# Optimization experiments

Hardware: AMD Instinct MI355X
Metric: run time of the kernel (lower is better)

The kernel has to match this reference:

```python
import jax, jax.numpy as jnp
import numpy as np

B, T, DM, H, DK, DV = 2, 2048, 1024, 16, 64, 64


def setup_inputs() -> dict:
    key = jax.random.key(0)
    k = jax.random.split(key, 7)
    std_k = np.float32(1.0 / np.sqrt(DK))
    std_v = np.float32(1.0 / np.sqrt(DV))
    return {
        "xq": jax.random.normal(k[0], (B, T, DM), jnp.float32),
        "xk": jax.random.normal(k[1], (B, T, DM), jnp.float32),
        "xv": jax.random.normal(k[2], (B, T, DM), jnp.float32),
        "mask": jnp.ones((B, T), jnp.float32),  # padding mask: 1 = keep
        "w_q": jax.random.normal(k[3], (H, DM, DK), jnp.float32) * std_k,
        "w_k": jax.random.normal(k[4], (H, DM, DK), jnp.float32) * std_k,
        "w_v": jax.random.normal(k[5], (H, DM, DV), jnp.float32) * std_v,
        "w_o": jax.random.normal(k[6], (H * DV, DM), jnp.float32) * np.float32(1.0 / np.sqrt(H * DV)),
        "b_o": jnp.zeros((DM,), jnp.float32),
    }


def reference(xq, xk, xv, mask, w_q, w_k, w_v, w_o, b_o):
    d_k = w_q.shape[-1]
    # per-head projections: [B,T,DM] x [H,DM,DK] -> [B,H,T,DK]
    q = jnp.einsum('bsd,hdk->bhsk', xq, w_q)
    kk = jnp.einsum('btd,hdk->bhtk', xk, w_k)
    v = jnp.einsum('btd,hdv->bhtv', xv, w_v)
    # NOTE: source divides by d_k (not sqrt(d_k)) -- kept faithful
    scores = jnp.einsum('bhsk,bhtk->bhst', q, kk) / jnp.float32(d_k)
    # _padding_mask: multiply by mask broadcast over key dim, then any exact
    # zero (masked OR coincidentally zero score) becomes -inf -- kept faithful
    masked = scores * mask[:, None, None, :]
    scores = jnp.where(masked == 0.0, -jnp.inf, masked)
    attn = jax.nn.softmax(scores, axis=-1)
    out = jnp.einsum('bhst,bhtv->bhsv', attn, v)  # [B,H,T,DV]
    b, h, t, dv = out.shape
    concat = out.transpose(0, 2, 1, 3).reshape(b, t, h * dv)
    return concat @ w_o + b_o
```

## Files before the change

### kernel.cpp

```cpp
#include <hip/hip_runtime.h>
#include <hip/hip_bf16.h>


typedef __attribute__((ext_vector_type(8))) short short8;
typedef __attribute__((ext_vector_type(4))) short short4v;
typedef __attribute__((ext_vector_type(4))) float f32x4;
typedef __attribute__((ext_vector_type(4))) int i32x4;

__device__ __forceinline__ short f2bf(float f) {
  union { float f; unsigned u; } v; v.f = f;
  unsigned r = v.u + 0x7FFFu + ((v.u >> 16) & 1u);
  return (short)(r >> 16);
}

#define GLD_LDS(g, l) __builtin_amdgcn_global_load_lds( \
    (const __attribute__((address_space(1))) void*)(g), \
    (__attribute__((address_space(3))) void*)(l), 16, 0, 0)

__global__ __launch_bounds__(256) void prep_all(
    const float* __restrict__ xq, const float* __restrict__ xk,
    const float* __restrict__ xv, const float* __restrict__ wq,
    const float* __restrict__ wk, const float* __restrict__ wv,
    const float* __restrict__ wo,
    short* __restrict__ Xb, short* __restrict__ Wall, short* __restrict__ Wot)
{
  const int bx = blockIdx.x, tid = threadIdx.x;
  __shared__ float Lt[64][65];
  if (bx < 6144) {
    int z = bx >> 11;
    const float* x = z == 0 ? xq : (z == 1 ? xk : xv);
    size_t i = ((size_t)(bx & 2047) * 256 + tid) * 8;
    f32x4 f0 = *(const f32x4*)(x + i);
    f32x4 f1 = *(const f32x4*)(x + i + 4);
    short8 s;
#pragma unroll
    for (int j = 0; j < 4; j++) { s[j] = f2bf(f0[j]); s[4 + j] = f2bf(f1[j]); }
    *(short8*)(Xb + (size_t)z * 4194304 + i) = s;
  } else if (bx < 6912) {
    int bz = bx - 6144;
    int z = bz >> 8, inner = bz & 255;
    const float* w = z == 0 ? wq : (z == 1 ? wk : wv);
    short* Wt = Wall + (size_t)z * 1048576;
    int h = inner >> 4, d0 = (inner & 15) * 64;
#pragma unroll
    for (int it = 0; it < 4; it++) {
      int e = tid + it * 256;
      int dl = e >> 4, k4 = (e & 15) * 4;
      f32x4 v = *(const f32x4*)(w + ((size_t)(h * 1024 + d0 + dl) * 64) + k4);
#pragma unroll
      for (int j = 0; j < 4; j++) Lt[dl][k4 + j] = v[j];
    }
    __syncthreads();
#pragma unroll
    for (int it = 0; it < 4; it++) {
      int e = tid + it * 256;
      int kl = e >> 4, dq = e & 15;
      short4v s;
#pragma unroll
      for (int j = 0; j < 4; j++) s[j] = f2bf(Lt[dq * 4 + j][kl]);
      *(short4v*)(Wt + (size_t)(h * 64 + kl) * 1024 + d0 + dq * 4) = s;
    }
  } else {
    int bz = bx - 6912;
    int k0 = (bz >> 4) * 64, n0 = (bz & 15) * 64;
#pragma unroll
    for (int it = 0; it < 4; it++) {
      int e = tid + it * 256;
      int kl = e >> 4, n4 = (e & 15) * 4;
      f32x4 v = *(const f32x4*)(wo + (size_t)(k0 + kl) * 1024 + n0 + n4);
#pragma unroll
      for (int j = 0; j < 4; j++) Lt[kl][n4 + j] = v[j];
    }
    __syncthreads();
#pragma unroll
    for (int it = 0; it < 4; it++) {
      int e = tid + it * 256;
      int nl = e >> 4, kq = e & 15;
      short4v s;
#pragma unroll
      for (int j = 0; j < 4; j++) s[j] = f2bf(Lt[kq * 4 + j][nl]);
      *(short4v*)(Wot + (size_t)(n0 + nl) * 1024 + k0 + kq * 4) = s;
    }
  }
}

__global__ __launch_bounds__(256) void proj_qkv2(
    const short* __restrict__ Xb, const short* __restrict__ Wall,
    short* __restrict__ Qb, short* __restrict__ Kt2, short* __restrict__ Vt2)
{
  const int z = blockIdx.z;
  const short* X  = Xb   + (size_t)z * 4194304;
  const short* Wt = Wall + (size_t)z * 1048576;

  const int t0 = blockIdx.x * 128;
  const int n0 = blockIdx.y * 128;
  const int tid = threadIdx.x, w = tid >> 6, lane = tid & 63;
  const int c = lane & 15, q4 = lane >> 4;
  const int wn = (w & 1) * 64, wt = (w >> 1) * 64;
  const int srow = lane >> 2, scol = (lane & 3) * 8;

  __shared__ __align__(16) short Al[128 * 32];
  __shared__ __align__(16) short Bl[128 * 32];

  f32x4 acc[4][4] = {};

  for (int k0 = 0; k0 < 1024; k0 += 32) {
#pragma unroll
    for (int i = 0; i < 2; i++) {
      int rg = (w * 2 + i) * 16;
      GLD_LDS(Wt + (size_t)(n0 + rg + srow) * 1024 + k0 + scol, Al + rg * 32);
      GLD_LDS(X  + (size_t)(t0 + rg + srow) * 1024 + k0 + scol, Bl + rg * 32);
    }
    __syncthreads();
    short8 a[4], bfr[4];
#pragma unroll
    for (int i = 0; i < 4; i++)
      a[i] = *(const short8*)(Al + (wn + i * 16 + c) * 32 + q4 * 8);
#pragma unroll
    for (int j = 0; j < 4; j++)
      bfr[j] = *(const short8*)(Bl + (wt + j * 16 + c) * 32 + q4 * 8);
#pragma unroll
    for (int i = 0; i < 4; i++)
#pragma unroll
      for (int j = 0; j < 4; j++)
        acc[i][j] = __builtin_amdgcn_mfma_f32_16x16x32_bf16(a[i], bfr[j], acc[i][j], 0, 0, 0);
    __syncthreads();
  }

#pragma unroll
  for (int i = 0; i < 4; i++)
#pragma unroll
    for (int j = 0; j < 4; j++) {
      int n = n0 + wn + i * 16 + q4 * 4;
      int trow = t0 + wt + j * 16 + c;
      int b = trow >> 11, t = trow & 2047;
      int h = n >> 6, cc = n & 63;
      int bh = b * 16 + h;
      f32x4 v = acc[i][j];
      short4v pk;
#pragma unroll
      for (int r = 0; r < 4; r++) pk[r] = f2bf(v[r]);
      if (z == 0) {
        *(short4v*)(Qb + (size_t)(bh * 2048 + t) * 64 + cc) = pk;
      } else if (z == 1) {
        int t5 = t & 31, s_ = t5 >> 4, c_ = t5 & 15;
        size_t base = (size_t)bh * 131072 + (t >> 5) * 2048;
#pragma unroll
        for (int r = 0; r < 4; r++) {
          int dv = cc + r;
          Kt2[base + ((s_ * 2 + (dv >> 5)) * 16 + c_) * 32 + ((dv >> 3) & 3) * 8 + (dv & 7)] = pk[r];
        }
      } else {
        int t5 = t & 31;
        int kp = ((t5 >> 2) & 3) * 8 + ((t5 >> 4) & 1) * 4 + (t5 & 3);
        size_t base = (size_t)bh * 131072 + (t >> 5) * 2048;
#pragma unroll
        for (int r = 0; r < 4; r++)
          Vt2[base + (size_t)(cc + r) * 32 + kp] = pk[r];
      }
    }
}

__global__ __launch_bounds__(256, 2) void attn5(
    const short* __restrict__ Qb, const short* __restrict__ Kt2,
    const short* __restrict__ Vt2, const float* __restrict__ mask,
    short* __restrict__ AO)
{
  const int tblk = blockIdx.x;
  const int bh = blockIdx.y;
  const int b = bh >> 4, h = bh & 15;
  const short* Qh = Qb  + (size_t)bh * 131072;
  const short* Kh = Kt2 + (size_t)bh * 131072;
  const short* Vh = Vt2 + (size_t)bh * 131072;

  const int tid = threadIdx.x, w = tid >> 6, lane = tid & 63;
  const int c = lane & 15, q4 = lane >> 4;
  const int qrow0 = tblk * 128 + w * 32;

  short8 qa[2][2];
#pragma unroll
  for (int u = 0; u < 2; u++)
#pragma unroll
    for (int dc = 0; dc < 2; dc++)
      qa[u][dc] = *(const short8*)(Qh + (size_t)(qrow0 + u * 16 + c) * 64 + dc * 32 + q4 * 8);

  f32x4 acc[2][4] = {};
  float l[2] = {0.f, 0.f};
  const float LOG2E_64 = 1.44269504088896f * 0.015625f;

  const short* kP = Kh + c * 32 + q4 * 8;
  const short* vP = Vh + c * 32 + q4 * 8;
  const float* mP = mask + b * 2048 + q4 * 4;

  short8 kf0[2][2], kf1[2][2], va0[4], va1[4];

#define PREF(KF, VA) do { \
    KF[0][0] = *(const short8*)(kP);        KF[0][1] = *(const short8*)(kP + 512); \
    KF[1][0] = *(const short8*)(kP + 1024); KF[1][1] = *(const short8*)(kP + 1536); \
    VA[0] = *(const short8*)(vP);        VA[1] = *(const short8*)(vP + 512); \
    VA[2] = *(const short8*)(vP + 1024); VA[3] = *(const short8*)(vP + 1536); \
    kP += 2048; vP += 2048; \
  } while (0)

#define BODY(KF, VA) do { \
    f32x4 st[2][2] = {}; \
    _Pragma("unroll") \
    for (int u = 0; u < 2; u++) \
      _Pragma("unroll") \
      for (int s = 0; s < 2; s++) { \
        st[u][s] = __builtin_amdgcn_mfma_f32_16x16x32_bf16(KF[s][0], qa[u][0], st[u][s], 0, 0, 0); \
        st[u][s] = __builtin_amdgcn_mfma_f32_16x16x32_bf16(KF[s][1], qa[u][1], st[u][s], 0, 0, 0); \
      } \
    f32x4 cm[2], cb[2]; \
    _Pragma("unroll") \
    for (int s = 0; s < 2; s++) { \
      f32x4 mk = *(const f32x4*)(mP + s * 16); \
      cm[s] = mk * LOG2E_64; \
      cb[s] = (mk - 1.0f) * 240.0f; \
    } \
    mP += 32; \
    _Pragma("unroll") \
    for (int u = 0; u < 2; u++) { \
      unsigned pkd[2][2]; \
      _Pragma("unroll") \
      for (int s = 0; s < 2; s++) { \
        float e0 = __builtin_amdgcn_exp2f(st[u][s][0] * cm[s][0] + cb[s][0]); \
        float e1 = __builtin_amdgcn_exp2f(st[u][s][1] * cm[s][1] + cb[s][1]); \
        float e2 = __builtin_amdgcn_exp2f(st[u][s][2] * cm[s][2] + cb[s][2]); \
        float e3 = __builtin_amdgcn_exp2f(st[u][s][3] * cm[s][3] + cb[s][3]); \
        l[u] += (e0 + e1) + (e2 + e3); \
        union { float f; unsigned u; } a0, a1, a2, a3; \
        a0.f = e0; a1.f = e1; a2.f = e2; a3.f = e3; \
        pkd[s][0] = __builtin_amdgcn_perm(a1.u + 0x8000u, a0.u + 0x8000u, 0x07060302u); \
        pkd[s][1] = __builtin_amdgcn_perm(a3.u + 0x8000u, a2.u + 0x8000u, 0x07060302u); \
      } \
      union { i32x4 i; short8 s; } pb; \
      pb.i[0] = (int)pkd[0][0]; pb.i[1] = (int)pkd[0][1]; \
      pb.i[2] = (int)pkd[1][0]; pb.i[3] = (int)pkd[1][1]; \
      _Pragma("unroll") \
      for (int vs = 0; vs < 4; vs++) \
        acc[u][vs] = __builtin_amdgcn_mfma_f32_16x16x32_bf16(VA[vs], pb.s, acc[u][vs], 0, 0, 0); \
    } \
  } while (0)

  PREF(kf0, va0);
  for (int ii = 0; ii < 32; ii++) {
    PREF(kf1, va1);
    BODY(kf0, va0);
    if (ii < 31) PREF(kf0, va0);
    BODY(kf1, va1);
  }
#undef PREF
#undef BODY

#pragma unroll
  for (int u = 0; u < 2; u++) {
    float lu = l[u];
    lu += __shfl_xor(lu, 16);
    lu += __shfl_xor(lu, 32);
    float inv = 1.0f / lu;
    size_t row = (size_t)b * 2048 + qrow0 + u * 16 + c;
#pragma unroll
    for (int vs = 0; vs < 4; vs++) {
      f32x4 v = acc[u][vs];
      short4v pk;
#pragma unroll
      for (int r = 0; r < 4; r++) pk[r] = f2bf(v[r] * inv);
      *(short4v*)(AO + row * 1024 + h * 64 + vs * 16 + q4 * 4) = pk;
    }
  }
}

__global__ __launch_bounds__(256) void out_proj2(
    const short* __restrict__ AO, const short* __restrict__ Wot,
    const float* __restrict__ bo, float* __restrict__ out)
{
  const int t0 = blockIdx.x * 128;
  const int n0 = blockIdx.y * 128;
  const int tid = threadIdx.x, w = tid >> 6, lane = tid & 63;
  const int c = lane & 15, q4 = lane >> 4;
  const int wn = (w & 1) * 64, wt = (w >> 1) * 64;
  const int srow = lane >> 2, scol = (lane & 3) * 8;

  __shared__ __align__(16) short Al[128 * 32];
  __shared__ __align__(16) short Bl[128 * 32];

  f32x4 acc[4][4] = {};

  for (int k0 = 0; k0 < 1024; k0 += 32) {
#pragma unroll
    for (int i = 0; i < 2; i++) {
      int rg = (w * 2 + i) * 16;
      GLD_LDS(Wot + (size_t)(n0 + rg + srow) * 1024 + k0 + scol, Al + rg * 32);
      GLD_LDS(AO  + (size_t)(t0 + rg + srow) * 1024 + k0 + scol, Bl + rg * 32);
    }
    __syncthreads();
    short8 a[4], bfr[4];
#pragma unroll
    for (int i = 0; i < 4; i++)
      a[i] = *(const short8*)(Al + (wn + i * 16 + c) * 32 + q4 * 8);
#pragma unroll
    for (int j = 0; j < 4; j++)
      bfr[j] = *(const short8*)(Bl + (wt + j * 16 + c) * 32 + q4 * 8);
#pragma unroll
    for (int i = 0; i < 4; i++)
#pragma unroll
      for (int j = 0; j < 4; j++)
        acc[i][j] = __builtin_amdgcn_mfma_f32_16x16x32_bf16(a[i], bfr[j], acc[i][j], 0, 0, 0);
    __syncthreads();
  }

#pragma unroll
  for (int i = 0; i < 4; i++)
#pragma unroll
    for (int j = 0; j < 4; j++) {
      int n = n0 + wn + i * 16 + q4 * 4;
      int trow = t0 + wt + j * 16 + c;
      f32x4 v = acc[i][j] + *(const f32x4*)(bo + n);
      *(f32x4*)(out + (size_t)trow * 1024 + n) = v;
    }
}

extern "C" void kernel_launch(void* const* d_in, const int* in_sizes, int n_in,
                              void* d_out, int out_size, void* d_ws, size_t ws_size,
                              hipStream_t stream)
{
  (void)in_sizes; (void)n_in; (void)out_size; (void)ws_size;
  const float* xq   = (const float*)d_in[0];
  const float* xk   = (const float*)d_in[1];
  const float* xv   = (const float*)d_in[2];
  const float* mask = (const float*)d_in[3];
  const float* wq   = (const float*)d_in[4];
  const float* wk   = (const float*)d_in[5];
  const float* wv   = (const float*)d_in[6];
  const float* wo   = (const float*)d_in[7];
  const float* bo   = (const float*)d_in[8];
  float* out = (float*)d_out;

  char* ws = (char*)d_ws;
  short* Wall = (short*)(ws + (size_t)0);
  short* Wot  = (short*)(ws + ((size_t)6 << 20));
  short* Xb   = (short*)(ws + ((size_t)8 << 20));
  short* AO   = (short*)(ws + ((size_t)8 << 20));
  short* Qb   = (short*)(ws + ((size_t)32 << 20));
  short* Kt2  = (short*)(ws + ((size_t)40 << 20));
  short* Vt2  = (short*)(ws + ((size_t)48 << 20));

  prep_all<<<7168, 256, 0, stream>>>(xq, xk, xv, wq, wk, wv, wo, Xb, Wall, Wot);
  proj_qkv2<<<dim3(32, 8, 3), 256, 0, stream>>>(Xb, Wall, Qb, Kt2, Vt2);
  attn5<<<dim3(16, 32), 256, 0, stream>>>(Qb, Kt2, Vt2, mask, AO);
  out_proj2<<<dim3(32, 8), 256, 0, stream>>>(AO, Wot, bo, out);
}
```

Measured before the change: 244.7 us.

## Split attention key range across warps and reduce partial sums in LDS

Each block now handles 32 query rows instead of 128, and its four warps each process a quarter of the key sequence for the same rows, so the grid grows from 512 to 2048 blocks. Partial accumulators and row sums are combined through shared memory by warp 0. This works only because the softmax uses no running max (fixed scaling), so the partial sums add directly. The aim is more parallelism and occupancy (launch bounds raised to 4 blocks per SIMD group), at the cost of an LDS reduction, a barrier, and reloading K/V per block four times as often.

```diff
diff --git a/kernel.cpp b/kernel.cpp
--- a/kernel.cpp
+++ b/kernel.cpp
@@ -161,7 +161,7 @@
     }
 }
 
-__global__ __launch_bounds__(256, 2) void attn5(
+__global__ __launch_bounds__(256, 4) void attn5(
     const short* __restrict__ Qb, const short* __restrict__ Kt2,
     const short* __restrict__ Vt2, const float* __restrict__ mask,
     short* __restrict__ AO)
@@ -175,7 +175,7 @@
 
   const int tid = threadIdx.x, w = tid >> 6, lane = tid & 63;
   const int c = lane & 15, q4 = lane >> 4;
-  const int qrow0 = tblk * 128 + w * 32;
+  const int qrow0 = tblk * 32;
 
   short8 qa[2][2];
 #pragma unroll
@@ -188,9 +188,9 @@
   float l[2] = {0.f, 0.f};
   const float LOG2E_64 = 1.44269504088896f * 0.015625f;
 
-  const short* kP = Kh + c * 32 + q4 * 8;
-  const short* vP = Vh + c * 32 + q4 * 8;
-  const float* mP = mask + b * 2048 + q4 * 4;
+  const short* kP = Kh + (size_t)w * 16 * 2048 + c * 32 + q4 * 8;
+  const short* vP = Vh + (size_t)w * 16 * 2048 + c * 32 + q4 * 8;
+  const float* mP = mask + b * 2048 + w * 512 + q4 * 4;
 
   short8 kf0[2][2], kf1[2][2], va0[4], va1[4];
 
@@ -244,29 +244,53 @@
   } while (0)
 
   PREF(kf0, va0);
-  for (int ii = 0; ii < 32; ii++) {
+  for (int ii = 0; ii < 8; ii++) {
     PREF(kf1, va1);
     BODY(kf0, va0);
-    if (ii < 31) PREF(kf0, va0);
+    if (ii < 7) PREF(kf0, va0);
     BODY(kf1, va1);
   }
 #undef PREF
 #undef BODY
 
-#pragma unroll
-  for (int u = 0; u < 2; u++) {
-    float lu = l[u];
-    lu += __shfl_xor(lu, 16);
-    lu += __shfl_xor(lu, 32);
-    float inv = 1.0f / lu;
-    size_t row = (size_t)b * 2048 + qrow0 + u * 16 + c;
-#pragma unroll
-    for (int vs = 0; vs < 4; vs++) {
-      f32x4 v = acc[u][vs];
-      short4v pk;
-#pragma unroll
-      for (int r = 0; r < 4; r++) pk[r] = f2bf(v[r] * inv);
-      *(short4v*)(AO + row * 1024 + h * 64 + vs * 16 + q4 * 4) = pk;
+  __shared__ __align__(16) float Cmb[3][64][34];
+  if (w > 0) {
+    float* dst = &Cmb[w - 1][lane][0];
+#pragma unroll
+    for (int u = 0; u < 2; u++)
+#pragma unroll
+      for (int vs = 0; vs < 4; vs++)
+        *(f32x4*)(dst + u * 16 + vs * 4) = acc[u][vs];
+    dst[32] = l[0]; dst[33] = l[1];
+  }
+  __syncthreads();
+  if (w == 0) {
+#pragma unroll
+    for (int ww = 0; ww < 3; ww++) {
+      const float* src = &Cmb[ww][lane][0];
+#pragma unroll
+      for (int u = 0; u < 2; u++)
+#pragma unroll
+        for (int vs = 0; vs < 4; vs++)
+          acc[u][vs] += *(const f32x4*)(src + u * 16 + vs * 4);
+      l[0] += src[32]; l[1] += src[33];
+    }
+
+#pragma unroll
+    for (int u = 0; u < 2; u++) {
+      float lu = l[u];
+      lu += __shfl_xor(lu, 16);
+      lu += __shfl_xor(lu, 32);
+      float inv = 1.0f / lu;
+      size_t row = (size_t)b * 2048 + qrow0 + u * 16 + c;
+#pragma unroll
+      for (int vs = 0; vs < 4; vs++) {
+        f32x4 v = acc[u][vs];
+        short4v pk;
+#pragma unroll
+        for (int r = 0; r < 4; r++) pk[r] = f2bf(v[r] * inv);
+        *(short4v*)(AO + row * 1024 + h * 64 + vs * 16 + q4 * 4) = pk;
+      }
     }
   }
 }
@@ -348,6 +372,6 @@
 
   prep_all<<<7168, 256, 0, stream>>>(xq, xk, xv, wq, wk, wv, wo, Xb, Wall, Wot);
   proj_qkv2<<<dim3(32, 8, 3), 256, 0, stream>>>(Xb, Wall, Qb, Kt2, Vt2);
-  attn5<<<dim3(16, 32), 256, 0, stream>>>(Qb, Kt2, Vt2, mask, AO);
+  attn5<<<dim3(64, 32), 256, 0, stream>>>(Qb, Kt2, Vt2, mask, AO);
   out_proj2<<<dim3(32, 8), 256, 0, stream>>>(AO, Wot, bo, out);
 }
```

Measured after the change: 246.0 us. No clear change (+0.5%).

## Share K/V tiles across waves via double-buffered LDS with direct global-to-LDS loads

Applied to the files above, without the earlier changes.

The attention kernel used to have each of its four waves load the same K and V tiles from global memory into registers on its own. Now each wave stages one eighth-slice of the shared 32-key K/V tile into a double-buffered LDS array using global_load_lds, with an XOR swizzle to avoid bank conflicts. All waves then read their MFMA fragments from LDS. This cuts redundant global/L2 traffic by about four times, but adds a vmcnt wait and a block barrier on every iteration, plus LDS reads.

```diff
diff --git a/kernel.cpp b/kernel.cpp
--- a/kernel.cpp
+++ b/kernel.cpp
@@ -161,7 +161,7 @@
     }
 }
 
-__global__ __launch_bounds__(256, 2) void attn5(
+__global__ __launch_bounds__(256, 2) void attn7(
     const short* __restrict__ Qb, const short* __restrict__ Kt2,
     const short* __restrict__ Vt2, const float* __restrict__ mask,
     short* __restrict__ AO)
@@ -177,6 +177,12 @@
   const int c = lane & 15, q4 = lane >> 4;
   const int qrow0 = tblk * 128 + w * 32;
 
+  __shared__ __align__(16) short KV[2][4096];
+
+  const int ch = c * 4 + q4;
+  const int rdo = (ch ^ ((ch >> 3) & 3)) * 8;
+  const int sch = (lane ^ ((lane >> 3) & 3)) * 8;
+
   short8 qa[2][2];
 #pragma unroll
   for (int u = 0; u < 2; u++)
@@ -187,29 +193,34 @@
   f32x4 acc[2][4] = {};
   float l[2] = {0.f, 0.f};
   const float LOG2E_64 = 1.44269504088896f * 0.015625f;
-
-  const short* kP = Kh + c * 32 + q4 * 8;
-  const short* vP = Vh + c * 32 + q4 * 8;
   const float* mP = mask + b * 2048 + q4 * 4;
 
-  short8 kf0[2][2], kf1[2][2], va0[4], va1[4];
-
-#define PREF(KF, VA) do { \
-    KF[0][0] = *(const short8*)(kP);        KF[0][1] = *(const short8*)(kP + 512); \
-    KF[1][0] = *(const short8*)(kP + 1024); KF[1][1] = *(const short8*)(kP + 1536); \
-    VA[0] = *(const short8*)(vP);        VA[1] = *(const short8*)(vP + 512); \
-    VA[2] = *(const short8*)(vP + 1024); VA[3] = *(const short8*)(vP + 1536); \
-    kP += 2048; vP += 2048; \
+  const int g0 = w * 2;
+
+#define STAGE(BUF, T) do { \
+    const short* sb = (g0 < 4) ? (Kh + (size_t)(T) * 2048 + g0 * 512) \
+                               : (Vh + (size_t)(T) * 2048 + (g0 - 4) * 512); \
+    GLD_LDS(sb + sch,        &KV[BUF][g0 * 512]); \
+    GLD_LDS(sb + 512 + sch,  &KV[BUF][g0 * 512 + 512]); \
   } while (0)
 
-#define BODY(KF, VA) do { \
+#define BODY(BUF) do { \
+    short8 kf[2][2], va[4]; \
+    _Pragma("unroll") \
+    for (int s = 0; s < 2; s++) \
+      _Pragma("unroll") \
+      for (int dc = 0; dc < 2; dc++) \
+        kf[s][dc] = *(const short8*)(&KV[BUF][(s * 2 + dc) * 512 + rdo]); \
+    _Pragma("unroll") \
+    for (int vs = 0; vs < 4; vs++) \
+      va[vs] = *(const short8*)(&KV[BUF][(4 + vs) * 512 + rdo]); \
     f32x4 st[2][2] = {}; \
     _Pragma("unroll") \
     for (int u = 0; u < 2; u++) \
       _Pragma("unroll") \
       for (int s = 0; s < 2; s++) { \
-        st[u][s] = __builtin_amdgcn_mfma_f32_16x16x32_bf16(KF[s][0], qa[u][0], st[u][s], 0, 0, 0); \
-        st[u][s] = __builtin_amdgcn_mfma_f32_16x16x32_bf16(KF[s][1], qa[u][1], st[u][s], 0, 0, 0); \
+        st[u][s] = __builtin_amdgcn_mfma_f32_16x16x32_bf16(kf[s][0], qa[u][0], st[u][s], 0, 0, 0); \
+        st[u][s] = __builtin_amdgcn_mfma_f32_16x16x32_bf16(kf[s][1], qa[u][1], st[u][s], 0, 0, 0); \
       } \
     f32x4 cm[2], cb[2]; \
     _Pragma("unroll") \
@@ -239,18 +250,23 @@
       pb.i[2] = (int)pkd[1][0]; pb.i[3] = (int)pkd[1][1]; \
       _Pragma("unroll") \
       for (int vs = 0; vs < 4; vs++) \
-        acc[u][vs] = __builtin_amdgcn_mfma_f32_16x16x32_bf16(VA[vs], pb.s, acc[u][vs], 0, 0, 0); \
+        acc[u][vs] = __builtin_amdgcn_mfma_f32_16x16x32_bf16(va[vs], pb.s, acc[u][vs], 0, 0, 0); \
     } \
   } while (0)
 
-  PREF(kf0, va0);
-  for (int ii = 0; ii < 32; ii++) {
-    PREF(kf1, va1);
-    BODY(kf0, va0);
-    if (ii < 31) PREF(kf0, va0);
-    BODY(kf1, va1);
-  }
-#undef PREF
+  STAGE(0, 0);
+  asm volatile("s_waitcnt vmcnt(0)" ::: "memory");
+  __syncthreads();
+  int cur = 0;
+  for (int t = 0; t < 63; ++t) {
+    STAGE(cur ^ 1, t + 1);
+    BODY(cur);
+    asm volatile("s_waitcnt vmcnt(0)" ::: "memory");
+    __syncthreads();
+    cur ^= 1;
+  }
+  BODY(cur);
+#undef STAGE
 #undef BODY
 
 #pragma unroll
@@ -348,6 +364,6 @@
 
   prep_all<<<7168, 256, 0, stream>>>(xq, xk, xv, wq, wk, wv, wo, Xb, Wall, Wot);
   proj_qkv2<<<dim3(32, 8, 3), 256, 0, stream>>>(Xb, Wall, Qb, Kt2, Vt2);
-  attn5<<<dim3(16, 32), 256, 0, stream>>>(Qb, Kt2, Vt2, mask, AO);
+  attn7<<<dim3(16, 32), 256, 0, stream>>>(Qb, Kt2, Vt2, mask, AO);
   out_proj2<<<dim3(32, 8), 256, 0, stream>>>(AO, Wot, bo, out);
 }
```

Measured after the change: 228.3 us. 1.07x faster.
